# Kernel optimization log

Measured on AMD Instinct MI355X. Metric: run time of the kernel, lower is better.

Reference implementation:

```python
import jax, jax.numpy as jnp
import numpy as np
import math

EMBED = 1024
HEADS = 16
DHEAD = 64
B, S = 2, 2048


def setup_inputs() -> dict:
    key = jax.random.key(0)
    k1, k2, k3, k4 = jax.random.split(key, 4)
    qs = jax.random.normal(k1, (B, S, EMBED), dtype=jnp.float32)
    # causal mask, broadcast over batch (mask==0 positions are masked out)
    mask = jnp.broadcast_to(jnp.tril(jnp.ones((S, S), dtype=jnp.int32)), (B, S, S))
    # torch Linear(embed, 3*H*D, bias=False): y = x @ W^T; store transposed [E, 3HD]
    Wqkv = jax.random.normal(k2, (EMBED, 3 * HEADS * DHEAD), dtype=jnp.float32) / math.sqrt(EMBED)
    Wout = jax.random.normal(k3, (HEADS * DHEAD, EMBED), dtype=jnp.float32) / math.sqrt(HEADS * DHEAD)
    bout = jax.random.normal(k4, (EMBED,), dtype=jnp.float32) * 0.01
    return {"qs": qs, "mask": mask, "Wqkv": Wqkv, "Wout": Wout, "bout": bout}


def reference(qs, mask, Wqkv, Wout, bout):
    b, s, _ = qs.shape
    # fused QKV projection -> (B, S, 3H, D), split into q/k/v chunks of H heads
    qkv = (qs @ Wqkv).reshape(b, s, 3 * HEADS, DHEAD)
    q, k, v = qkv[:, :, :HEADS], qkv[:, :, HEADS:2 * HEADS], qkv[:, :, 2 * HEADS:]
    # scores: (B, H, Sq, Sk)
    scores = jnp.einsum("bqhd,bkhd->bhqk", q, k) / math.sqrt(DHEAD)
    scores = jnp.where(mask[:, None, :, :] == 0, jnp.float32(-1e9), scores)
    attn = jax.nn.softmax(scores, axis=-1)
    out = jnp.einsum("bhqk,bkhd->bqhd", attn, v).reshape(b, s, HEADS * DHEAD)
    return out @ Wout + bout
```

## Files before the change

kernel.cpp:

```cpp
#include <hip/hip_runtime.h>
#include <hip/hip_bf16.h>
#include <stdint.h>


typedef __attribute__((ext_vector_type(8))) short  short8;
typedef __attribute__((ext_vector_type(4))) short  short4v;
typedef __attribute__((ext_vector_type(4))) float  float4v;

#define SOFTMAX_BIAS 17.3123405f

__device__ __forceinline__ unsigned short f2bf(float f) {
  unsigned int u = __builtin_bit_cast(unsigned int, f);
  u += 0x7fffu + ((u >> 16) & 1u);
  return (unsigned short)(u >> 16);
}

__device__ __forceinline__ void async_copy16(const void* g, void* l) {
  __builtin_amdgcn_global_load_lds(
      (__attribute__((address_space(1))) unsigned int*)g,
      (__attribute__((address_space(3))) unsigned int*)l, 16, 0, 0);
}

__global__ void cvt_bf16_kernel(const float* __restrict__ in,
                                unsigned short* __restrict__ out, int n) {
  int i = (blockIdx.x * 256 + threadIdx.x) * 4;
  if (i < n) {
    float4v v = *(const float4v*)(in + i);
    short4v o;
    o[0] = (short)f2bf(v[0]); o[1] = (short)f2bf(v[1]);
    o[2] = (short)f2bf(v[2]); o[3] = (short)f2bf(v[3]);
    *(short4v*)(out + i) = o;
  }
}

__global__ void transpose_cvt_kernel(const float* __restrict__ W,
                                     unsigned short* __restrict__ Wt,
                                     int K, int N) {
  __shared__ float t[32][33];
  const int x = threadIdx.x, y = threadIdx.y;
  const int n0 = blockIdx.x * 32, k0 = blockIdx.y * 32;
#pragma unroll
  for (int i = 0; i < 4; ++i)
    t[y + i * 8][x] = W[(size_t)(k0 + y + i * 8) * N + n0 + x];
  __syncthreads();
#pragma unroll
  for (int i = 0; i < 4; ++i)
    Wt[(size_t)(n0 + y + i * 8) * K + k0 + x] = f2bf(t[x][y + i * 8]);
}

__device__ __forceinline__ void gemm_bt_core(const unsigned short* __restrict__ A,
                                             const unsigned short* __restrict__ Bt,
                                             int m0, int n0,
                                             short* As, short* Bs,
                                             float4v (&acc)[4][4],
                                             int wm, int wn, int l15, int quad,
                                             int tid) {
  for (int k0 = 0; k0 < 1024; k0 += 32) {
    __syncthreads();
#pragma unroll
    for (int i = 0; i < 2; ++i) {
      int u = i * 256 + tid;
      int r = u >> 2, cpw = u & 3;
      int c = cpw ^ ((r >> 1) & 3);
      async_copy16(A  + (size_t)(m0 + r) * 1024 + k0 + c * 8, As + u * 8);
      async_copy16(Bt + (size_t)(n0 + r) * 1024 + k0 + c * 8, Bs + u * 8);
    }
    __syncthreads();

    short8 af[4], bfv[4];
#pragma unroll
    for (int t = 0; t < 4; ++t) {
      int ra = wm * 64 + t * 16 + l15;
      af[t]  = *(const short8*)(As + (ra * 4 + (quad ^ ((ra >> 1) & 3))) * 8);
      int rb = wn * 64 + t * 16 + l15;
      bfv[t] = *(const short8*)(Bs + (rb * 4 + (quad ^ ((rb >> 1) & 3))) * 8);
    }
#pragma unroll
    for (int mt = 0; mt < 4; ++mt)
#pragma unroll
      for (int nt = 0; nt < 4; ++nt)
        acc[mt][nt] = __builtin_amdgcn_mfma_f32_16x16x32_bf16(
            af[mt], bfv[nt], acc[mt][nt], 0, 0, 0);
  }
}

__global__ __launch_bounds__(256, 3)
void gemm_qkv_kernel(const unsigned short* __restrict__ Aq,
                     const unsigned short* __restrict__ Bt,
                     unsigned short* __restrict__ Qb,
                     unsigned short* __restrict__ Kb,
                     unsigned short* __restrict__ Vb) {
  __shared__ short As[128 * 32];
  __shared__ short Bs[128 * 32];
  const int tid = threadIdx.x, lane = tid & 63, w = tid >> 6;
  const int wm = w & 1, wn = w >> 1, l15 = lane & 15, quad = lane >> 4;
  const int m0 = blockIdx.x * 128, n0 = blockIdx.y * 128;

  float4v acc[4][4];
#pragma unroll
  for (int i = 0; i < 4; ++i)
#pragma unroll
    for (int j = 0; j < 4; ++j) acc[i][j] = (float4v)0.0f;

  gemm_bt_core(Aq, Bt, m0, n0, As, Bs, acc, wm, wn, l15, quad, tid);

#pragma unroll
  for (int nt = 0; nt < 4; ++nt) {
    int gn = n0 + wn * 64 + nt * 16 + l15;
    int j = gn >> 6, d = gn & 63;
    int g = j >> 4, h = j & 15;
#pragma unroll
    for (int mt = 0; mt < 4; ++mt) {
#pragma unroll
      for (int r = 0; r < 4; ++r) {
        int gm = m0 + wm * 64 + mt * 16 + quad * 4 + r;
        int b = gm >> 11, s = gm & 2047;
        float v = acc[mt][nt][r];
        if (g == 0)
          Qb[(((size_t)(b * 16 + h) * 2048 + s) << 6) + d] = f2bf(v * 0.18033688f);
        else if (g == 1)
          Kb[(((size_t)(b * 16 + h) * 2048 + s) << 6) + d] = f2bf(v);
        else
          Vb[(((size_t)(b * 16 + h) * 64 + d) << 11) + s] = f2bf(v);
      }
    }
  }
}

__global__ __launch_bounds__(256, 2)
void flash_attn_kernel(const unsigned short* __restrict__ Qb,
                       const unsigned short* __restrict__ Kb,
                       const unsigned short* __restrict__ Vb,
                       unsigned short* __restrict__ Ob) {
  __shared__ unsigned short Kt[128 * 64];
  __shared__ unsigned short Vt[64 * 128];
  __shared__ unsigned short Pl[4][32 * 80];

  const int tid = threadIdx.x, lane = tid & 63, w = tid >> 6;
  const int l15 = lane & 15, quad = lane >> 4;
  const int qt = 15 - blockIdx.x;
  const int bh = blockIdx.y;
  const int bb = bh >> 4, h = bh & 15;

  const unsigned short* Qg = Qb + (size_t)bh * 2048 * 64;
  const unsigned short* Kg = Kb + (size_t)bh * 2048 * 64;
  const unsigned short* Vg = Vb + (size_t)bh * 64 * 2048;
  unsigned short* Pw = &Pl[w][0];

  const int qb0 = qt * 128 + w * 32;

  short8 qf[2][2];
#pragma unroll
  for (int nt = 0; nt < 2; ++nt)
#pragma unroll
    for (int kc = 0; kc < 2; ++kc)
      qf[nt][kc] = *(const short8*)(Qg + (size_t)(qb0 + nt * 16 + l15) * 64 +
                                    kc * 32 + quad * 8);

  float l_s[2] = {0.0f, 0.0f};
  float4v o[4][2];
#pragma unroll
  for (int i = 0; i < 4; ++i) { o[i][0] = (float4v)0.0f; o[i][1] = (float4v)0.0f; }

  for (int kt = 0; kt <= qt; ++kt) {
    const int kb = kt * 128;
    __syncthreads();
#pragma unroll
    for (int i = 0; i < 4; ++i) {
      int u = i * 256 + tid;
      int r = u >> 3, cp = u & 7;
      async_copy16(Kg + (size_t)(kb + r) * 64 + (cp ^ (r & 7)) * 8, Kt + u * 8);
      int r2 = u >> 4, cp2 = u & 15;
      async_copy16(Vg + (size_t)r2 * 2048 + kb + (cp2 ^ (r2 & 15)) * 8, Vt + u * 8);
    }
    __syncthreads();

    float4v st[8][2];
#pragma unroll
    for (int mt = 0; mt < 8; ++mt) {
      st[mt][0] = (float4v)(-SOFTMAX_BIAS);
      st[mt][1] = (float4v)(-SOFTMAX_BIAS);
      int key = mt * 16 + l15;
#pragma unroll
      for (int kc = 0; kc < 2; ++kc) {
        int cp = (kc * 4 + quad) ^ (key & 7);
        short8 a = *(const short8*)(Kt + key * 64 + cp * 8);
        st[mt][0] = __builtin_amdgcn_mfma_f32_16x16x32_bf16(a, qf[0][kc], st[mt][0], 0, 0, 0);
        st[mt][1] = __builtin_amdgcn_mfma_f32_16x16x32_bf16(a, qf[1][kc], st[mt][1], 0, 0, 0);
      }
    }

    if (kt == qt) {
#pragma unroll
      for (int nt = 0; nt < 2; ++nt) {
        int qg = qb0 + nt * 16 + l15;
#pragma unroll
        for (int mt = 0; mt < 8; ++mt)
#pragma unroll
          for (int r = 0; r < 4; ++r) {
            int keyg = kb + mt * 16 + quad * 4 + r;
            if (keyg > qg) st[mt][nt][r] = -1e5f;
          }
      }
    }

#pragma unroll
    for (int nt = 0; nt < 2; ++nt) {
      float sum = 0.0f;
#pragma unroll
      for (int mt = 0; mt < 8; ++mt)
#pragma unroll
        for (int r = 0; r < 4; ++r) {
          float p = __builtin_amdgcn_exp2f(st[mt][nt][r]);
          st[mt][nt][r] = p;
          sum += p;
        }
      sum += __shfl_xor(sum, 16);
      sum += __shfl_xor(sum, 32);
      l_s[nt] += sum;
    }

#pragma unroll
    for (int hf = 0; hf < 2; ++hf) {
#pragma unroll
      for (int nt = 0; nt < 2; ++nt) {
        int ql = nt * 16 + l15;
        unsigned short* prow = Pw + ql * 80;
#pragma unroll
        for (int mtl = 0; mtl < 4; ++mtl) {
          int mt = hf * 4 + mtl;
          short4v pk;
          pk[0] = (short)f2bf(st[mt][nt][0]); pk[1] = (short)f2bf(st[mt][nt][1]);
          pk[2] = (short)f2bf(st[mt][nt][2]); pk[3] = (short)f2bf(st[mt][nt][3]);
          int cp = (mtl * 2 + (quad >> 1)) ^ (l15 & 7);
          *(short4v*)(prow + cp * 8 + (quad & 1) * 4) = pk;
        }
      }
#pragma unroll
      for (int kcl = 0; kcl < 2; ++kcl) {
        int kcg = hf * 2 + kcl;
        short8 pb[2];
#pragma unroll
        for (int nt = 0; nt < 2; ++nt) {
          int ql = nt * 16 + l15;
          int cp = (kcl * 4 + quad) ^ (l15 & 7);
          pb[nt] = *(const short8*)(Pw + ql * 80 + cp * 8);
        }
#pragma unroll
        for (int mtd = 0; mtd < 4; ++mtd) {
          int d = mtd * 16 + l15;
          int cp2 = (kcg * 4 + quad) ^ (d & 15);
          short8 a = *(const short8*)(Vt + d * 128 + cp2 * 8);
          o[mtd][0] = __builtin_amdgcn_mfma_f32_16x16x32_bf16(a, pb[0], o[mtd][0], 0, 0, 0);
          o[mtd][1] = __builtin_amdgcn_mfma_f32_16x16x32_bf16(a, pb[1], o[mtd][1], 0, 0, 0);
        }
      }
    }
  }

#pragma unroll
  for (int nt = 0; nt < 2; ++nt) {
    float inv = 1.0f / l_s[nt];
    int qg = qb0 + nt * 16 + l15;
#pragma unroll
    for (int mtd = 0; mtd < 4; ++mtd) {
      short4v pk;
      pk[0] = (short)f2bf(o[mtd][nt][0] * inv);
      pk[1] = (short)f2bf(o[mtd][nt][1] * inv);
      pk[2] = (short)f2bf(o[mtd][nt][2] * inv);
      pk[3] = (short)f2bf(o[mtd][nt][3] * inv);
      *(short4v*)(Ob + (size_t)(bb * 2048 + qg) * 1024 + h * 64 + mtd * 16 +
                  quad * 4) = pk;
    }
  }
}

__global__ __launch_bounds__(256, 3)
void gemm_out_kernel(const unsigned short* __restrict__ Aq,
                     const unsigned short* __restrict__ Bt,
                     const float* __restrict__ bout,
                     float* __restrict__ out) {
  __shared__ short As[64 * 32];
  __shared__ short Bs[128 * 32];
  const int tid = threadIdx.x, lane = tid & 63, w = tid >> 6;
  const int wm = w & 1, wn = w >> 1, l15 = lane & 15, quad = lane >> 4;
  const int m0 = blockIdx.x * 64, n0 = blockIdx.y * 128;

  float4v acc[2][4];
#pragma unroll
  for (int i = 0; i < 2; ++i)
#pragma unroll
    for (int j = 0; j < 4; ++j) acc[i][j] = (float4v)0.0f;

  for (int k0 = 0; k0 < 1024; k0 += 32) {
    __syncthreads();
    {
      int u = tid;
      int r = u >> 2, cpw = u & 3;
      int c = cpw ^ ((r >> 1) & 3);
      async_copy16(Aq + (size_t)(m0 + r) * 1024 + k0 + c * 8, As + u * 8);
    }
#pragma unroll
    for (int i = 0; i < 2; ++i) {
      int u = i * 256 + tid;
      int r = u >> 2, cpw = u & 3;
      int c = cpw ^ ((r >> 1) & 3);
      async_copy16(Bt + (size_t)(n0 + r) * 1024 + k0 + c * 8, Bs + u * 8);
    }
    __syncthreads();

    short8 af[2], bfv[4];
#pragma unroll
    for (int t = 0; t < 2; ++t) {
      int ra = wm * 32 + t * 16 + l15;
      af[t] = *(const short8*)(As + (ra * 4 + (quad ^ ((ra >> 1) & 3))) * 8);
    }
#pragma unroll
    for (int t = 0; t < 4; ++t) {
      int rb = wn * 64 + t * 16 + l15;
      bfv[t] = *(const short8*)(Bs + (rb * 4 + (quad ^ ((rb >> 1) & 3))) * 8);
    }
#pragma unroll
    for (int mt = 0; mt < 2; ++mt)
#pragma unroll
      for (int nt = 0; nt < 4; ++nt)
        acc[mt][nt] = __builtin_amdgcn_mfma_f32_16x16x32_bf16(
            af[mt], bfv[nt], acc[mt][nt], 0, 0, 0);
  }

#pragma unroll
  for (int nt = 0; nt < 4; ++nt) {
    int gn = n0 + wn * 64 + nt * 16 + l15;
    float bias = bout[gn];
#pragma unroll
    for (int mt = 0; mt < 2; ++mt) {
      int gmb = m0 + wm * 32 + mt * 16 + quad * 4;
#pragma unroll
      for (int r = 0; r < 4; ++r)
        out[(size_t)(gmb + r) * 1024 + gn] = acc[mt][nt][r] + bias;
    }
  }
}

extern "C" void kernel_launch(void* const* d_in, const int* in_sizes, int n_in,
                              void* d_out, int out_size, void* d_ws, size_t ws_size,
                              hipStream_t stream) {
  (void)in_sizes; (void)n_in; (void)out_size; (void)ws_size;
  const float* qs   = (const float*)d_in[0];
  const float* Wqkv = (const float*)d_in[2];
  const float* Wout = (const float*)d_in[3];
  const float* bout = (const float*)d_in[4];
  float* out = (float*)d_out;

  unsigned short* qs_bf = (unsigned short*)d_ws;
  unsigned short* WqkvT = qs_bf + 4096 * 1024;
  unsigned short* WoutT = WqkvT + 3072 * 1024;
  unsigned short* Qb    = WoutT + 1024 * 1024;
  unsigned short* Kb    = Qb + 32 * 2048 * 64;
  unsigned short* Vb    = Kb + 32 * 2048 * 64;
  unsigned short* Ob    = Vb + 32 * 2048 * 64;

  cvt_bf16_kernel<<<4096, 256, 0, stream>>>(qs, qs_bf, 4096 * 1024);
  transpose_cvt_kernel<<<dim3(96, 32), dim3(32, 8), 0, stream>>>(Wqkv, WqkvT, 1024, 3072);
  transpose_cvt_kernel<<<dim3(32, 32), dim3(32, 8), 0, stream>>>(Wout, WoutT, 1024, 1024);
  gemm_qkv_kernel<<<dim3(32, 24), 256, 0, stream>>>(qs_bf, WqkvT, Qb, Kb, Vb);
  flash_attn_kernel<<<dim3(16, 32), 256, 0, stream>>>(Qb, Kb, Vb, Ob);
  gemm_out_kernel<<<dim3(64, 8), 256, 0, stream>>>(Ob, WoutT, bout, out);
}
```

Baseline: 211.4 us.

## Split flash attention over key range and merge halves in a combine kernel

Each query tile's key loop is split across two blocks (split-K), doubling the attention grid so the causal workload spreads across more CUs. Unnormalized partial outputs and row sums go to reused workspace buffers, and a new combine kernel adds the two halves and normalizes. The three prep kernels are merged into one launch, and P conversion uses truncation instead of round-to-nearest. This adds an extra pass over the output and a bf16 rounding of the partials. It relies on the fixed softmax bias rather than a running max, so the partials can be summed directly.

Result: no change. 209.4 us (-0.9%).

```diff
diff --git a/kernel.cpp b/kernel.cpp
--- a/kernel.cpp
+++ b/kernel.cpp
@@ -14,6 +14,13 @@
   u += 0x7fffu + ((u >> 16) & 1u);
   return (unsigned short)(u >> 16);
 }
+__device__ __forceinline__ unsigned short f2bf_trunc(float f) {
+  return (unsigned short)(__builtin_bit_cast(unsigned int, f) >> 16);
+}
+__device__ __forceinline__ float bf2f(unsigned short s) {
+  unsigned int u = ((unsigned int)s) << 16;
+  return __builtin_bit_cast(float, u);
+}
 
 __device__ __forceinline__ void async_copy16(const void* g, void* l) {
   __builtin_amdgcn_global_load_lds(
@@ -21,31 +28,36 @@
       (__attribute__((address_space(3))) unsigned int*)l, 16, 0, 0);
 }
 
-__global__ void cvt_bf16_kernel(const float* __restrict__ in,
-                                unsigned short* __restrict__ out, int n) {
-  int i = (blockIdx.x * 256 + threadIdx.x) * 4;
-  if (i < n) {
-    float4v v = *(const float4v*)(in + i);
+__global__ void prep_kernel(const float* __restrict__ qs,
+                            const float* __restrict__ Wqkv,
+                            const float* __restrict__ Wout,
+                            unsigned short* __restrict__ qs_bf,
+                            unsigned short* __restrict__ WqkvT,
+                            unsigned short* __restrict__ WoutT) {
+  __shared__ float tbuf[32][33];
+  const int blk = blockIdx.x, tid = threadIdx.x;
+  if (blk < 4096) {
+    int i = (blk * 256 + tid) * 4;
+    float4v v = *(const float4v*)(qs + i);
     short4v o;
     o[0] = (short)f2bf(v[0]); o[1] = (short)f2bf(v[1]);
     o[2] = (short)f2bf(v[2]); o[3] = (short)f2bf(v[3]);
-    *(short4v*)(out + i) = o;
-  }
-}
-
-__global__ void transpose_cvt_kernel(const float* __restrict__ W,
-                                     unsigned short* __restrict__ Wt,
-                                     int K, int N) {
-  __shared__ float t[32][33];
-  const int x = threadIdx.x, y = threadIdx.y;
-  const int n0 = blockIdx.x * 32, k0 = blockIdx.y * 32;
-#pragma unroll
-  for (int i = 0; i < 4; ++i)
-    t[y + i * 8][x] = W[(size_t)(k0 + y + i * 8) * N + n0 + x];
-  __syncthreads();
-#pragma unroll
-  for (int i = 0; i < 4; ++i)
-    Wt[(size_t)(n0 + y + i * 8) * K + k0 + x] = f2bf(t[x][y + i * 8]);
+    *(short4v*)(qs_bf + i) = o;
+  } else {
+    const float* W; unsigned short* Wt; int N, t;
+    if (blk < 4096 + 3072) { W = Wqkv; Wt = WqkvT; N = 3072; t = blk - 4096; }
+    else                   { W = Wout; Wt = WoutT; N = 1024; t = blk - 7168; }
+    const int tilesx = N >> 5;
+    const int n0 = (t % tilesx) * 32, k0 = (t / tilesx) * 32;
+    const int x = tid & 31, y = tid >> 5;
+#pragma unroll
+    for (int i = 0; i < 4; ++i)
+      tbuf[y + i * 8][x] = W[(size_t)(k0 + y + i * 8) * N + n0 + x];
+    __syncthreads();
+#pragma unroll
+    for (int i = 0; i < 4; ++i)
+      Wt[(size_t)(n0 + y + i * 8) * 1024 + k0 + x] = f2bf(tbuf[x][y + i * 8]);
+  }
 }
 
 __device__ __forceinline__ void gemm_bt_core(const unsigned short* __restrict__ A,
@@ -131,16 +143,23 @@
 void flash_attn_kernel(const unsigned short* __restrict__ Qb,
                        const unsigned short* __restrict__ Kb,
                        const unsigned short* __restrict__ Vb,
-                       unsigned short* __restrict__ Ob) {
+                       unsigned short* __restrict__ Pp0,
+                       unsigned short* __restrict__ Pp1,
+                       float* __restrict__ lws) {
   __shared__ unsigned short Kt[128 * 64];
   __shared__ unsigned short Vt[64 * 128];
   __shared__ unsigned short Pl[4][32 * 80];
 
   const int tid = threadIdx.x, lane = tid & 63, w = tid >> 6;
   const int l15 = lane & 15, quad = lane >> 4;
-  const int qt = 15 - blockIdx.x;
+  const int qt = 15 - (blockIdx.x >> 1);
+  const int half = blockIdx.x & 1;
   const int bh = blockIdx.y;
   const int bb = bh >> 4, h = bh & 15;
+
+  const int n = qt + 1, nh0 = (n + 1) >> 1;
+  const int kt_lo = half ? nh0 : 0;
+  const int kt_hi = half ? n : nh0;
 
   const unsigned short* Qg = Qb + (size_t)bh * 2048 * 64;
   const unsigned short* Kg = Kb + (size_t)bh * 2048 * 64;
@@ -162,7 +181,7 @@
 #pragma unroll
   for (int i = 0; i < 4; ++i) { o[i][0] = (float4v)0.0f; o[i][1] = (float4v)0.0f; }
 
-  for (int kt = 0; kt <= qt; ++kt) {
+  for (int kt = kt_lo; kt < kt_hi; ++kt) {
     const int kb = kt * 128;
     __syncthreads();
 #pragma unroll
@@ -230,8 +249,10 @@
         for (int mtl = 0; mtl < 4; ++mtl) {
           int mt = hf * 4 + mtl;
           short4v pk;
-          pk[0] = (short)f2bf(st[mt][nt][0]); pk[1] = (short)f2bf(st[mt][nt][1]);
-          pk[2] = (short)f2bf(st[mt][nt][2]); pk[3] = (short)f2bf(st[mt][nt][3]);
+          pk[0] = (short)f2bf_trunc(st[mt][nt][0]);
+          pk[1] = (short)f2bf_trunc(st[mt][nt][1]);
+          pk[2] = (short)f2bf_trunc(st[mt][nt][2]);
+          pk[3] = (short)f2bf_trunc(st[mt][nt][3]);
           int cp = (mtl * 2 + (quad >> 1)) ^ (l15 & 7);
           *(short4v*)(prow + cp * 8 + (quad & 1) * 4) = pk;
         }
@@ -258,21 +279,40 @@
     }
   }
 
+  unsigned short* Pp = half ? Pp1 : Pp0;
 #pragma unroll
   for (int nt = 0; nt < 2; ++nt) {
-    float inv = 1.0f / l_s[nt];
     int qg = qb0 + nt * 16 + l15;
+    if (quad == 0) lws[half * 65536 + bh * 2048 + qg] = l_s[nt];
 #pragma unroll
     for (int mtd = 0; mtd < 4; ++mtd) {
       short4v pk;
-      pk[0] = (short)f2bf(o[mtd][nt][0] * inv);
-      pk[1] = (short)f2bf(o[mtd][nt][1] * inv);
-      pk[2] = (short)f2bf(o[mtd][nt][2] * inv);
-      pk[3] = (short)f2bf(o[mtd][nt][3] * inv);
-      *(short4v*)(Ob + (size_t)(bb * 2048 + qg) * 1024 + h * 64 + mtd * 16 +
+      pk[0] = (short)f2bf(o[mtd][nt][0]);
+      pk[1] = (short)f2bf(o[mtd][nt][1]);
+      pk[2] = (short)f2bf(o[mtd][nt][2]);
+      pk[3] = (short)f2bf(o[mtd][nt][3]);
+      *(short4v*)(Pp + (size_t)(bb * 2048 + qg) * 1024 + h * 64 + mtd * 16 +
                   quad * 4) = pk;
     }
   }
+}
+
+__global__ void combine_kernel(const unsigned short* __restrict__ P0,
+                               unsigned short* __restrict__ P1,
+                               const float* __restrict__ lws) {
+  int idx = (blockIdx.x * 256 + threadIdx.x) * 8;
+  int t = idx >> 10, c = idx & 1023;
+  int bh = (t >> 11) * 16 + (c >> 6);
+  int q = t & 2047;
+  float inv = 1.0f / (lws[bh * 2048 + q] + lws[65536 + bh * 2048 + q]);
+  short8 a = *(const short8*)(P0 + idx);
+  short8 b = *(const short8*)(P1 + idx);
+  short8 r;
+#pragma unroll
+  for (int j = 0; j < 8; ++j)
+    r[j] = (short)f2bf((bf2f((unsigned short)a[j]) +
+                        bf2f((unsigned short)b[j])) * inv);
+  *(short8*)(P1 + idx) = r;
 }
 
 __global__ __launch_bounds__(256, 3)
@@ -360,10 +400,13 @@
   unsigned short* Vb    = Kb + 32 * 2048 * 64;
   unsigned short* Ob    = Vb + 32 * 2048 * 64;
 
-  cvt_bf16_kernel<<<4096, 256, 0, stream>>>(qs, qs_bf, 4096 * 1024);
-  transpose_cvt_kernel<<<dim3(96, 32), dim3(32, 8), 0, stream>>>(Wqkv, WqkvT, 1024, 3072);
-  transpose_cvt_kernel<<<dim3(32, 32), dim3(32, 8), 0, stream>>>(Wout, WoutT, 1024, 1024);
+  unsigned short* P0 = qs_bf;
+  float*          lw = (float*)WqkvT;
+  unsigned short* P1 = Ob;
+
+  prep_kernel<<<8192, 256, 0, stream>>>(qs, Wqkv, Wout, qs_bf, WqkvT, WoutT);
   gemm_qkv_kernel<<<dim3(32, 24), 256, 0, stream>>>(qs_bf, WqkvT, Qb, Kb, Vb);
-  flash_attn_kernel<<<dim3(16, 32), 256, 0, stream>>>(Qb, Kb, Vb, Ob);
-  gemm_out_kernel<<<dim3(64, 8), 256, 0, stream>>>(Ob, WoutT, bout, out);
-}
+  flash_attn_kernel<<<dim3(32, 32), 256, 0, stream>>>(Qb, Kb, Vb, P0, P1, lw);
+  combine_kernel<<<2048, 256, 0, stream>>>(P0, P1, lw);
+  gemm_out_kernel<<<dim3(64, 8), 256, 0, stream>>>(P1, WoutT, bout, out);
+}
```
